# Kernel optimization log

Measured on AMD Instinct MI355X. Metric: run time of the kernel, lower is better.

## Reference

```python
import jax, jax.numpy as jnp
import numpy as np

B, H, W = 16, 288, 384
NUM_ITER = 5      # LMSolver num_iter
LM_DAMP = 1e-4
Z_MIN = 0.01      # PerspectiveCamera z_min
REL_DELTA = 0.1   # AdaptiveHuberPnPCost relative_delta


def skew(v):
    x, y, z = v[..., 0], v[..., 1], v[..., 2]
    O = jnp.zeros_like(x)
    return jnp.stack([jnp.stack([O, -z, y], -1),
                      jnp.stack([z, O, -x], -1),
                      jnp.stack([-y, x, O], -1)], -2)


def exp_so3(w):
    th = jnp.maximum(jnp.linalg.norm(w, axis=-1, keepdims=True), 1e-8)
    K = skew(w / th)
    th = th[..., None]
    I = jnp.eye(3, dtype=w.dtype)
    return I + jnp.sin(th) * K + (1.0 - jnp.cos(th)) * (K @ K)


def se3_inv(T):
    R = T[..., :3, :3]
    t = T[..., :3, 3]
    Rt = jnp.swapaxes(R, -1, -2)
    ti = -jnp.einsum('...ij,...j->...i', Rt, t)
    return (jnp.zeros_like(T).at[..., :3, :3].set(Rt)
            .at[..., :3, 3].set(ti).at[..., 3, 3].set(1.0))


def project(x3d, R, t, K):
    Xc = jnp.einsum('bij,bnj->bni', R, x3d) + t[:, None]  # [B,N,3]
    z = jnp.maximum(Xc[..., 2], Z_MIN)
    fx, fy = K[:, 0, 0, None], K[:, 1, 1, None]
    cx, cy = K[:, 0, 2, None], K[:, 1, 2, None]
    uv = jnp.stack([fx * Xc[..., 0] / z + cx, fy * Xc[..., 1] / z + cy], -1)
    return uv, Xc


def lm_pnp(x3d, x2d, w2d, K):
    """Batched robust Levenberg-Marquardt PnP (replaces per-sample Python loop)."""
    Bb = x3d.shape[0]
    dt = x3d.dtype
    # AdaptiveHuberPnPCost.set_param: delta from spread of x2d
    delta = REL_DELTA * jnp.sqrt(jnp.var(x2d, axis=1).sum(-1))  # [B]
    R = jnp.broadcast_to(jnp.eye(3, dtype=dt), (Bb, 3, 3))
    t = jnp.zeros((Bb, 3), dt)
    I6 = jnp.eye(6, dtype=dt)
    for _ in range(NUM_ITER):
        uv, Xc = project(x3d, R, t, K)
        r = uv - x2d                           # [B,N,2]
        wr = w2d * r
        rn = jnp.linalg.norm(wr, axis=-1)      # [B,N]
        rob = jnp.sqrt(jnp.minimum(1.0, delta[:, None] / jnp.maximum(rn, 1e-8)))
        wt = w2d * rob[..., None]              # [B,N,2] Huber-IRLS weights
        z = jnp.maximum(Xc[..., 2], Z_MIN)
        iz = 1.0 / z
        fx, fy = K[:, 0, 0, None], K[:, 1, 1, None]
        zero = jnp.zeros_like(iz)
        Jp = jnp.stack([
            jnp.stack([fx * iz, zero, -fx * Xc[..., 0] * iz * iz], -1),
            jnp.stack([zero, fy * iz, -fy * Xc[..., 1] * iz * iz], -1)], -2)  # [B,N,2,3]
        Jrot = -jnp.einsum('bnij,bnjk->bnik', Jp, skew(Xc))
        J = jnp.concatenate([Jp, Jrot], -1)    # [B,N,2,6]
        Jw = J * wt[..., None]
        JTJ = jnp.einsum('bnif,bnig->bfg', Jw, Jw)
        JTr = jnp.einsum('bnif,bni->bf', Jw, wt * r)
        damp = LM_DAMP * jnp.trace(JTJ, axis1=-2, axis2=-1)[:, None, None] / 6.0 + 1e-6
        dx = -jnp.linalg.solve(JTJ + damp * I6, JTr[..., None])[..., 0]
        t = t + dx[:, :3]
        R = exp_so3(dx[:, 3:]) @ R
    T = (jnp.zeros((Bb, 4, 4), dt).at[:, :3, :3].set(R)
         .at[:, :3, 3].set(t).at[:, 3, 3].set(1.0))
    return T


def setup_inputs() -> dict:
    key = jax.random.key(0)
    k1, k2, k3, k4, k5 = jax.random.split(key, 5)
    f = 350.0
    Kmat = jnp.array([[f, 0.0, W / 2.0], [0.0, f, H / 2.0], [0.0, 0.0, 1.0]], jnp.float32)
    K = jnp.broadcast_to(Kmat, (B, 3, 3))
    # geometrically consistent points: backproject pixel grid with random depth
    xs = jnp.arange(W, dtype=jnp.float32)
    ys = jnp.arange(H, dtype=jnp.float32)
    gx, gy = jnp.meshgrid(xs, ys, indexing='xy')          # [H,W]
    depth = 2.0 + 4.0 * jax.random.uniform(k1, (B, H, W))
    X = (gx - W / 2.0) / f * depth
    Y = (gy - H / 2.0) / f * depth
    pts3d = jnp.stack([X, Y, depth], -1)
    pts3d = pts3d + 0.02 * jax.random.normal(k2, pts3d.shape)
    conf = 1.0 + jax.random.uniform(k3, (B, H, W))
    # valid SE(3) gt poses (small perturbations of identity)
    q = jax.random.normal(k4, (B, 4)) * 0.05
    q = q.at[:, 0].add(1.0)
    q = q / jnp.linalg.norm(q, axis=-1, keepdims=True)
    w_, x_, y_, z_ = q[:, 0], q[:, 1], q[:, 2], q[:, 3]
    Rg = jnp.stack([
        jnp.stack([1 - 2 * (y_**2 + z_**2), 2 * (x_ * y_ - z_ * w_), 2 * (x_ * z_ + y_ * w_)], -1),
        jnp.stack([2 * (x_ * y_ + z_ * w_), 1 - 2 * (x_**2 + z_**2), 2 * (y_ * z_ - x_ * w_)], -1),
        jnp.stack([2 * (x_ * z_ - y_ * w_), 2 * (y_ * z_ + x_ * w_), 1 - 2 * (x_**2 + y_**2)], -1)], -2)
    tg = 0.2 * jax.random.normal(k5, (B, 3))
    pose = (jnp.zeros((B, 4, 4), jnp.float32).at[:, :3, :3].set(Rg)
            .at[:, :3, 3].set(tg).at[:, 3, 3].set(1.0))
    return {'pts3d_in_other_view': pts3d.astype(jnp.float32),
            'conf': conf.astype(jnp.float32),
            'camera_intrinsics': K.astype(jnp.float32),
            'camera_pose': pose}


def reference(pts3d_in_other_view, conf, camera_intrinsics, camera_pose):
    Bb, Hh, Ww, _ = pts3d_in_other_view.shape
    N = Hh * Ww
    xs = jnp.arange(Ww, dtype=pts3d_in_other_view.dtype)
    ys = jnp.arange(Hh, dtype=pts3d_in_other_view.dtype)
    gx, gy = jnp.meshgrid(xs, ys, indexing='xy')
    pixels = jnp.stack([gx, gy], -1).reshape(1, N, 2)
    x3d = pts3d_in_other_view.reshape(Bb, N, 3)
    x2d = jnp.broadcast_to(pixels, (Bb, N, 2))
    w2d = jnp.broadcast_to(conf.reshape(Bb, N, 1), (Bb, N, 2))
    pred_poses = lm_pnp(x3d, x2d, w2d, camera_intrinsics)
    gt_rel = jnp.einsum('ij,bjk->bik', se3_inv(camera_pose[0]), camera_pose)
    pred_rel = jnp.einsum('ij,bjk->bik', se3_inv(pred_poses[0]), pred_poses)
    R_gt, R_pr = gt_rel[:, :3, :3], pred_rel[:, :3, :3]
    t_gt, t_pr = gt_rel[:, :3, 3], pred_rel[:, :3, 3]
    Rd = jnp.einsum('bji,bjk->bik', R_pr, R_gt)
    trace = Rd[:, 0, 0] + Rd[:, 1, 1] + Rd[:, 2, 2]
    cosang = jnp.clip(0.5 * (trace - 1.0), -1.0 + 1e-7, 1.0 - 1e-7)
    rot_loss = jnp.arccos(cosang).mean()
    trans_loss = jnp.linalg.norm(t_pr - t_gt, axis=-1).mean()
    return rot_loss + trans_loss, rot_loss, trans_loss
```

## Files before the change

kernel.cpp:

```cpp
#include <hip/hip_runtime.h>
#include <math.h>

#define NB 16
#define IMH 288
#define IMW 384
#define NPIX (IMH*IMW)
#define TPB 256
#define PPT 8
#define BPB (NPIX/(TPB*PPT))
#define NBLK (NB*BPB)
#define NITER 5

#define POSE_OFF 0
#define ACC_OFF (2*NB*12)
#define WS_DOUBLES (2*NB*12 + NITER*NB*27)

__device__ __forceinline__ void solve_updatef(const double* __restrict__ acc,
                                              const double* __restrict__ pin,
                                              float* __restrict__ Ro,
                                              double* __restrict__ to) {
    float A[6][6], rhs[6], inv[6];
    {
        int k = 0;
        #pragma unroll
        for (int f = 0; f < 6; f++) {
            #pragma unroll 6
            for (int g = f; g < 6; g++) {
                float v = (float)acc[k];
                A[f][g] = v; A[g][f] = v; k++;
            }
        }
    }
    #pragma unroll
    for (int f = 0; f < 6; f++) rhs[f] = -(float)acc[21 + f];

    float tr = A[0][0]+A[1][1]+A[2][2]+A[3][3]+A[4][4]+A[5][5];
    float damp = 1e-4f * tr * (1.0f/6.0f) + 1e-6f;
    #pragma unroll
    for (int f = 0; f < 6; f++) A[f][f] += damp;

    #pragma unroll
    for (int j = 0; j < 6; j++) {
        float s = A[j][j];
        #pragma unroll 6
        for (int m = 0; m < j; m++) s = fmaf(-A[j][m], A[j][m], s);
        float dd = __builtin_amdgcn_sqrtf(fmaxf(s, 1e-20f));
        A[j][j] = dd;
        inv[j] = __builtin_amdgcn_rcpf(dd);
        #pragma unroll 6
        for (int i = j + 1; i < 6; i++) {
            float s2 = A[i][j];
            #pragma unroll 6
            for (int m = 0; m < j; m++) s2 = fmaf(-A[i][m], A[j][m], s2);
            A[i][j] = s2 * inv[j];
        }
    }
    #pragma unroll
    for (int i = 0; i < 6; i++) {
        float s = rhs[i];
        #pragma unroll 6
        for (int m = 0; m < i; m++) s = fmaf(-A[i][m], rhs[m], s);
        rhs[i] = s * inv[i];
    }
    #pragma unroll
    for (int i = 5; i >= 0; i--) {
        float s = rhs[i];
        #pragma unroll 6
        for (int m = i + 1; m < 6; m++) s = fmaf(-A[m][i], rhs[m], s);
        rhs[i] = s * inv[i];
    }

    to[0] = pin[9]  + (double)rhs[0];
    to[1] = pin[10] + (double)rhs[1];
    to[2] = pin[11] + (double)rhs[2];

    float wx = rhs[3], wy = rhs[4], wz = rhs[5];
    float th = fmaxf(__builtin_amdgcn_sqrtf(fmaf(wx,wx,fmaf(wy,wy,wz*wz))), 1e-8f);
    float ith = __builtin_amdgcn_rcpf(th);
    float kx = wx*ith, ky = wy*ith, kz = wz*ith;
    float st, ctf;
    sincosf(th, &st, &ctf);
    float ct = 1.0f - ctf;
    float E[9];
    E[0] = 1.0f + ct*(kx*kx - 1.0f);
    E[1] = -st*kz + ct*kx*ky;
    E[2] =  st*ky + ct*kx*kz;
    E[3] =  st*kz + ct*ky*kx;
    E[4] = 1.0f + ct*(ky*ky - 1.0f);
    E[5] = -st*kx + ct*ky*kz;
    E[6] = -st*ky + ct*kz*kx;
    E[7] =  st*kx + ct*kz*ky;
    E[8] = 1.0f + ct*(kz*kz - 1.0f);

    float Rin[9];
    #pragma unroll
    for (int i = 0; i < 9; i++) Rin[i] = (float)pin[i];
    #pragma unroll
    for (int i = 0; i < 3; i++) {
        #pragma unroll
        for (int j = 0; j < 3; j++)
            Ro[i*3+j] = E[i*3+0]*Rin[0*3+j] + E[i*3+1]*Rin[1*3+j] + E[i*3+2]*Rin[2*3+j];
    }
}

__global__ void init_k(double* ws) {
    int i = threadIdx.x;
    for (int k = i; k < WS_DOUBLES; k += TPB) ws[k] = 0.0;
    __syncthreads();
    if (i < NB) {
        double* p = ws + POSE_OFF + i * 12;
        p[0] = 1.0; p[4] = 1.0; p[8] = 1.0;
    }
}

__global__ __launch_bounds__(TPB) void reduce_k(const float* __restrict__ x3d,
                                                const float* __restrict__ conf,
                                                const float* __restrict__ Kmat,
                                                double* __restrict__ ws, int it) {
    const int b = blockIdx.x / BPB;
    const int chunk = blockIdx.x % BPB;
    const int tid = threadIdx.x;

    const int ft = chunk * TPB + tid;
    const float4* P4 = reinterpret_cast<const float4*>(x3d + (size_t)b * NPIX * 3) + (size_t)ft * 6;
    const float4* W4 = reinterpret_cast<const float4*>(conf + (size_t)b * NPIX) + (size_t)ft * 2;
    const float4 va = P4[0], vb = P4[1], vc = P4[2], vd = P4[3], ve = P4[4], vf = P4[5];
    const float4 w0 = W4[0], w1 = W4[1];

    __shared__ double lds[TPB / 64][27];

    float R[9], t[3];
    if (it == 0) {
        R[0]=1.f; R[1]=0.f; R[2]=0.f;
        R[3]=0.f; R[4]=1.f; R[5]=0.f;
        R[6]=0.f; R[7]=0.f; R[8]=1.f;
        t[0]=t[1]=t[2]=0.f;
    } else {
        float Rn[9]; double tn[3];
        solve_updatef(ws + ACC_OFF + ((size_t)(it-1) * NB + b) * 27,
                      ws + POSE_OFF + (size_t)((it-1) & 1) * NB * 12 + (size_t)b * 12,
                      Rn, tn);
        #pragma unroll
        for (int i = 0; i < 9; i++) R[i] = Rn[i];
        t[0] = (float)tn[0]; t[1] = (float)tn[1]; t[2] = (float)tn[2];
        if (chunk == 0 && tid == 0) {
            double* pout = ws + POSE_OFF + (size_t)(it & 1) * NB * 12 + (size_t)b * 12;
            #pragma unroll
            for (int i = 0; i < 9; i++) pout[i] = (double)Rn[i];
            pout[9] = tn[0]; pout[10] = tn[1]; pout[11] = tn[2];
        }
    }

    const float fx = Kmat[b*9 + 0];
    const float fy = Kmat[b*9 + 4];
    const float cx = Kmat[b*9 + 2];
    const float cy = Kmat[b*9 + 5];
    const float delta = (float)(0.1 * sqrt(((double)(IMW*IMW - 1) + (double)(IMH*IMH - 1)) / 12.0));

    const int n0 = ft * PPT;
    const int v0 = n0 / IMW;
    const float cyv  = cy - (float)v0;
    const float cxu0 = cx - (float)(n0 - v0 * IMW);

    float ppx[8] = { va.x, va.w, vb.z, vc.y, vd.x, vd.w, ve.z, vf.y };
    float ppy[8] = { va.y, vb.x, vb.w, vc.z, vd.y, ve.x, ve.w, vf.z };
    float ppz[8] = { va.z, vb.y, vc.x, vc.w, vd.z, ve.y, vf.x, vf.w };
    float pw[8]  = { w0.x, w0.y, w0.z, w0.w, w1.x, w1.y, w1.z, w1.w };

    float facc[27];
    #pragma unroll
    for (int i = 0; i < 27; i++) facc[i] = 0.0f;

    #pragma unroll
    for (int g = 0; g < PPT; ++g) {
        float px = ppx[g], py = ppy[g], pz = ppz[g], w = pw[g];
        float u_off = cxu0 - (float)g;

        float Xx = fmaf(R[0], px, fmaf(R[1], py, fmaf(R[2], pz, t[0])));
        float Xy = fmaf(R[3], px, fmaf(R[4], py, fmaf(R[5], pz, t[1])));
        float Xz = fmaf(R[6], px, fmaf(R[7], py, fmaf(R[8], pz, t[2])));
        float z  = fmaxf(Xz, 0.01f);
        float iz = __builtin_amdgcn_rcpf(z);

        float Xxiz = Xx * iz, Xyiz = Xy * iz;
        float rx = fmaf(fx, Xxiz, u_off);
        float ry = fmaf(fy, Xyiz, cyv);

        float wrx = w * rx, wry = w * ry;
        float q  = fmaf(wrx, wrx, wry * wry);
        float rs = __builtin_amdgcn_rsqf(fmaxf(q, 1e-16f));
        float rob2 = fminf(1.0f, delta * rs);
        float sq = w * __builtin_amdgcn_sqrtf(rob2);

        float sqiz = sq * iz;
        float a  = fx * sqiz;
        float c  = fy * sqiz;
        float bb = -a * Xxiz;
        float d  = -c * Xyiz;

        float j0[6] = { a, 0.0f, bb,  bb*Xy,               fmaf(a, Xz, -bb*Xx), -a*Xy };
        float j1[6] = { 0.0f, c,  d,  fmaf(d, Xy, -c*Xz), -d*Xx,                 c*Xx };
        float rxs = sq * rx, rys = sq * ry;

        int k = 0;
        #pragma unroll
        for (int f = 0; f < 6; ++f) {
            #pragma unroll
            for (int gg = f; gg < 6; ++gg) {
                facc[k] += j0[f]*j0[gg] + j1[f]*j1[gg];
                k++;
            }
        }
        #pragma unroll
        for (int f = 0; f < 6; ++f)
            facc[21 + f] += j0[f]*rxs + j1[f]*rys;
    }

    int lane = tid & 63;
    int wave = tid >> 6;
    #pragma unroll
    for (int i = 0; i < 27; i++) {
        float v = facc[i];
        for (int off = 32; off > 0; off >>= 1) v += __shfl_down(v, off, 64);
        if (lane == 0) lds[wave][i] = (double)v;
    }
    __syncthreads();

    double* acc = ws + ACC_OFF + ((size_t)it * NB + b) * 27;
    if (tid < 27) {
        double v = 0.0;
        #pragma unroll
        for (int wv = 0; wv < TPB/64; wv++) v += lds[wv][tid];
        atomicAdd(acc + tid, v);
    }
}

__global__ __launch_bounds__(64) void loss_k(const double* __restrict__ ws,
                                             const float* __restrict__ pose,
                                             float* __restrict__ out) {
    int lane = threadIdx.x;
    double Rp[9] = {1,0,0, 0,1,0, 0,0,1}, tp[3] = {0,0,0};
    if (lane < NB) {
        float Rn[9]; double tn[3];
        solve_updatef(ws + ACC_OFF + ((size_t)(NITER-1) * NB + lane) * 27,
                      ws + POSE_OFF + (size_t)((NITER-1) & 1) * NB * 12 + (size_t)lane * 12,
                      Rn, tn);
        #pragma unroll
        for (int i = 0; i < 9; i++) Rp[i] = (double)Rn[i];
        tp[0] = tn[0]; tp[1] = tn[1]; tp[2] = tn[2];
    }
    double Rp0[9], tp0v[3];
    #pragma unroll
    for (int i = 0; i < 9; i++) Rp0[i] = __shfl(Rp[i], 0, 64);
    #pragma unroll
    for (int i = 0; i < 3; i++) tp0v[i] = __shfl(tp[i], 0, 64);

    double rot = 0.0, trans = 0.0;
    if (lane < NB) {
        const float* P0 = pose;
        const float* Pb = pose + lane * 16;
        double R0t[9];
        #pragma unroll
        for (int i = 0; i < 3; i++)
            #pragma unroll
            for (int j = 0; j < 3; j++) R0t[i*3+j] = (double)P0[j*4+i];
        double t0i[3];
        #pragma unroll
        for (int i = 0; i < 3; i++)
            t0i[i] = -(R0t[i*3+0]*P0[0*4+3] + R0t[i*3+1]*P0[1*4+3] + R0t[i*3+2]*P0[2*4+3]);
        double Rg[9], tg[3];
        #pragma unroll
        for (int i = 0; i < 3; i++) {
            #pragma unroll
            for (int j = 0; j < 3; j++)
                Rg[i*3+j] = R0t[i*3+0]*Pb[0*4+j] + R0t[i*3+1]*Pb[1*4+j] + R0t[i*3+2]*Pb[2*4+j];
            tg[i] = R0t[i*3+0]*Pb[0*4+3] + R0t[i*3+1]*Pb[1*4+3] + R0t[i*3+2]*Pb[2*4+3] + t0i[i];
        }
        double Rp0t[9];
        #pragma unroll
        for (int i = 0; i < 3; i++)
            #pragma unroll
            for (int j = 0; j < 3; j++) Rp0t[i*3+j] = Rp0[j*3+i];
        double tp0i[3];
        #pragma unroll
        for (int i = 0; i < 3; i++)
            tp0i[i] = -(Rp0t[i*3+0]*tp0v[0] + Rp0t[i*3+1]*tp0v[1] + Rp0t[i*3+2]*tp0v[2]);
        double Rr[9], tr[3];
        #pragma unroll
        for (int i = 0; i < 3; i++) {
            #pragma unroll
            for (int j = 0; j < 3; j++)
                Rr[i*3+j] = Rp0t[i*3+0]*Rp[0*3+j] + Rp0t[i*3+1]*Rp[1*3+j] + Rp0t[i*3+2]*Rp[2*3+j];
            tr[i] = Rp0t[i*3+0]*tp[0] + Rp0t[i*3+1]*tp[1] + Rp0t[i*3+2]*tp[2] + tp0i[i];
        }
        double trace = 0.0;
        #pragma unroll
        for (int i = 0; i < 3; i++)
            trace += Rr[0*3+i]*Rg[0*3+i] + Rr[1*3+i]*Rg[1*3+i] + Rr[2*3+i]*Rg[2*3+i];
        double cosang = 0.5 * (trace - 1.0);
        cosang = fmin(fmax(cosang, -1.0 + 1e-7), 1.0 - 1e-7);
        rot = acos(cosang);
        double d0 = tr[0]-tg[0], d1 = tr[1]-tg[1], d2 = tr[2]-tg[2];
        trans = sqrt(d0*d0 + d1*d1 + d2*d2);
    }
    for (int off = 8; off > 0; off >>= 1) {
        rot   += __shfl_down(rot, off, 64);
        trans += __shfl_down(trans, off, 64);
    }
    if (lane == 0) {
        rot /= NB; trans /= NB;
        out[0] = (float)(rot + trans);
        out[1] = (float)rot;
        out[2] = (float)trans;
    }
}

extern "C" void kernel_launch(void* const* d_in, const int* in_sizes, int n_in,
                              void* d_out, int out_size, void* d_ws, size_t ws_size,
                              hipStream_t stream) {
    const float* x3d  = (const float*)d_in[0];
    const float* conf = (const float*)d_in[1];
    const float* Kmat = (const float*)d_in[2];
    const float* pose = (const float*)d_in[3];
    float* out = (float*)d_out;
    double* ws = (double*)d_ws;

    hipLaunchKernelGGL(init_k, dim3(1), dim3(TPB), 0, stream, ws);
    for (int it = 0; it < NITER; ++it) {
        hipLaunchKernelGGL(reduce_k, dim3(NBLK), dim3(TPB), 0, stream,
                           x3d, conf, Kmat, ws, it);
    }
    hipLaunchKernelGGL(loss_k, dim3(1), dim3(64), 0, stream, ws, pose, out);
}
```

Measured before the change: 86.24 us.

## Fuse LM iterations into one persistent kernel with per-batch atomic readiness flags

Measured after the change: 305.4 us. +254.1%, slower.

```diff
diff --git a/kernel.cpp b/kernel.cpp
--- a/kernel.cpp
+++ b/kernel.cpp
@@ -11,14 +11,15 @@
 #define NBLK (NB*BPB)
 #define NITER 5
 
+#define PSTRIDE 16
+#define ASTRIDE 32
 #define POSE_OFF 0
-#define ACC_OFF (2*NB*12)
-#define WS_DOUBLES (2*NB*12 + NITER*NB*27)
+#define ACC_OFF ((NITER+1)*NB*PSTRIDE)
+#define WS_DOUBLES (ACC_OFF + NITER*NB*ASTRIDE)
 
 __device__ __forceinline__ void solve_updatef(const double* __restrict__ acc,
                                               const double* __restrict__ pin,
-                                              float* __restrict__ Ro,
-                                              double* __restrict__ to) {
+                                              double* __restrict__ pout) {
     float A[6][6], rhs[6], inv[6];
     {
         int k = 0;
@@ -70,9 +71,9 @@
         rhs[i] = s * inv[i];
     }
 
-    to[0] = pin[9]  + (double)rhs[0];
-    to[1] = pin[10] + (double)rhs[1];
-    to[2] = pin[11] + (double)rhs[2];
+    pout[9]  = pin[9]  + (double)rhs[0];
+    pout[10] = pin[10] + (double)rhs[1];
+    pout[11] = pin[11] + (double)rhs[2];
 
     float wx = rhs[3], wy = rhs[4], wz = rhs[5];
     float th = fmaxf(__builtin_amdgcn_sqrtf(fmaf(wx,wx,fmaf(wy,wy,wz*wz))), 1e-8f);
@@ -99,57 +100,39 @@
     for (int i = 0; i < 3; i++) {
         #pragma unroll
         for (int j = 0; j < 3; j++)
-            Ro[i*3+j] = E[i*3+0]*Rin[0*3+j] + E[i*3+1]*Rin[1*3+j] + E[i*3+2]*Rin[2*3+j];
+            pout[i*3+j] = (double)(E[i*3+0]*Rin[0*3+j] + E[i*3+1]*Rin[1*3+j] + E[i*3+2]*Rin[2*3+j]);
     }
 }
 
 __global__ void init_k(double* ws) {
     int i = threadIdx.x;
     for (int k = i; k < WS_DOUBLES; k += TPB) ws[k] = 0.0;
+    int* cnt = (int*)(ws + WS_DOUBLES);
+    for (int k = i; k < 2 * NITER * NB + 1; k += TPB) cnt[k] = 0;
     __syncthreads();
     if (i < NB) {
-        double* p = ws + POSE_OFF + i * 12;
+        double* p = ws + POSE_OFF + i * PSTRIDE;
         p[0] = 1.0; p[4] = 1.0; p[8] = 1.0;
     }
 }
 
-__global__ __launch_bounds__(TPB) void reduce_k(const float* __restrict__ x3d,
-                                                const float* __restrict__ conf,
-                                                const float* __restrict__ Kmat,
-                                                double* __restrict__ ws, int it) {
+__global__ __launch_bounds__(TPB) void fused_k(const float* __restrict__ x3d,
+                                               const float* __restrict__ conf,
+                                               const float* __restrict__ Kmat,
+                                               const float* __restrict__ pose,
+                                               float* __restrict__ out,
+                                               double* __restrict__ ws) {
     const int b = blockIdx.x / BPB;
     const int chunk = blockIdx.x % BPB;
     const int tid = threadIdx.x;
 
+    int* cnt     = (int*)(ws + WS_DOUBLES);
+    int* ready   = cnt + NITER * NB;
+    int* losscnt = ready + NITER * NB;
+
     const int ft = chunk * TPB + tid;
     const float4* P4 = reinterpret_cast<const float4*>(x3d + (size_t)b * NPIX * 3) + (size_t)ft * 6;
     const float4* W4 = reinterpret_cast<const float4*>(conf + (size_t)b * NPIX) + (size_t)ft * 2;
-    const float4 va = P4[0], vb = P4[1], vc = P4[2], vd = P4[3], ve = P4[4], vf = P4[5];
-    const float4 w0 = W4[0], w1 = W4[1];
-
-    __shared__ double lds[TPB / 64][27];
-
-    float R[9], t[3];
-    if (it == 0) {
-        R[0]=1.f; R[1]=0.f; R[2]=0.f;
-        R[3]=0.f; R[4]=1.f; R[5]=0.f;
-        R[6]=0.f; R[7]=0.f; R[8]=1.f;
-        t[0]=t[1]=t[2]=0.f;
-    } else {
-        float Rn[9]; double tn[3];
-        solve_updatef(ws + ACC_OFF + ((size_t)(it-1) * NB + b) * 27,
-                      ws + POSE_OFF + (size_t)((it-1) & 1) * NB * 12 + (size_t)b * 12,
-                      Rn, tn);
-        #pragma unroll
-        for (int i = 0; i < 9; i++) R[i] = Rn[i];
-        t[0] = (float)tn[0]; t[1] = (float)tn[1]; t[2] = (float)tn[2];
-        if (chunk == 0 && tid == 0) {
-            double* pout = ws + POSE_OFF + (size_t)(it & 1) * NB * 12 + (size_t)b * 12;
-            #pragma unroll
-            for (int i = 0; i < 9; i++) pout[i] = (double)Rn[i];
-            pout[9] = tn[0]; pout[10] = tn[1]; pout[11] = tn[2];
-        }
-    }
 
     const float fx = Kmat[b*9 + 0];
     const float fy = Kmat[b*9 + 4];
@@ -162,156 +145,187 @@
     const float cyv  = cy - (float)v0;
     const float cxu0 = cx - (float)(n0 - v0 * IMW);
 
-    float ppx[8] = { va.x, va.w, vb.z, vc.y, vd.x, vd.w, ve.z, vf.y };
-    float ppy[8] = { va.y, vb.x, vb.w, vc.z, vd.y, ve.x, ve.w, vf.z };
-    float ppz[8] = { va.z, vb.y, vc.x, vc.w, vd.z, ve.y, vf.x, vf.w };
-    float pw[8]  = { w0.x, w0.y, w0.z, w0.w, w1.x, w1.y, w1.z, w1.w };
-
-    float facc[27];
-    #pragma unroll
-    for (int i = 0; i < 27; i++) facc[i] = 0.0f;
-
-    #pragma unroll
-    for (int g = 0; g < PPT; ++g) {
-        float px = ppx[g], py = ppy[g], pz = ppz[g], w = pw[g];
-        float u_off = cxu0 - (float)g;
-
-        float Xx = fmaf(R[0], px, fmaf(R[1], py, fmaf(R[2], pz, t[0])));
-        float Xy = fmaf(R[3], px, fmaf(R[4], py, fmaf(R[5], pz, t[1])));
-        float Xz = fmaf(R[6], px, fmaf(R[7], py, fmaf(R[8], pz, t[2])));
-        float z  = fmaxf(Xz, 0.01f);
-        float iz = __builtin_amdgcn_rcpf(z);
-
-        float Xxiz = Xx * iz, Xyiz = Xy * iz;
-        float rx = fmaf(fx, Xxiz, u_off);
-        float ry = fmaf(fy, Xyiz, cyv);
-
-        float wrx = w * rx, wry = w * ry;
-        float q  = fmaf(wrx, wrx, wry * wry);
-        float rs = __builtin_amdgcn_rsqf(fmaxf(q, 1e-16f));
-        float rob2 = fminf(1.0f, delta * rs);
-        float sq = w * __builtin_amdgcn_sqrtf(rob2);
-
-        float sqiz = sq * iz;
-        float a  = fx * sqiz;
-        float c  = fy * sqiz;
-        float bb = -a * Xxiz;
-        float d  = -c * Xyiz;
-
-        float j0[6] = { a, 0.0f, bb,  bb*Xy,               fmaf(a, Xz, -bb*Xx), -a*Xy };
-        float j1[6] = { 0.0f, c,  d,  fmaf(d, Xy, -c*Xz), -d*Xx,                 c*Xx };
-        float rxs = sq * rx, rys = sq * ry;
-
-        int k = 0;
-        #pragma unroll
-        for (int f = 0; f < 6; ++f) {
+    __shared__ double lds[TPB / 64][27];
+    __shared__ int s_last, s_loss;
+
+    const int lane = tid & 63;
+    const int wave = tid >> 6;
+
+    for (int it = 0; it < NITER; ++it) {
+        if (it > 0) {
+            if (tid == 0) {
+                int spins = 0;
+                while (__hip_atomic_load(&ready[(it-1)*NB + b], __ATOMIC_ACQUIRE,
+                                         __HIP_MEMORY_SCOPE_AGENT) == 0) {
+                    __builtin_amdgcn_s_sleep(4);
+                    if (++spins > (1 << 27)) break;
+                }
+                __threadfence();
+            }
+            __syncthreads();
+        }
+
+        const double* pin = ws + POSE_OFF + ((size_t)it * NB + b) * PSTRIDE;
+        float R[9], t[3];
+        #pragma unroll
+        for (int i = 0; i < 9; i++) R[i] = (float)pin[i];
+        t[0] = (float)pin[9]; t[1] = (float)pin[10]; t[2] = (float)pin[11];
+
+        const float4 va = P4[0], vb = P4[1], vc = P4[2], vd = P4[3], ve = P4[4], vf = P4[5];
+        const float4 w0 = W4[0], w1 = W4[1];
+        float ppx[8] = { va.x, va.w, vb.z, vc.y, vd.x, vd.w, ve.z, vf.y };
+        float ppy[8] = { va.y, vb.x, vb.w, vc.z, vd.y, ve.x, ve.w, vf.z };
+        float ppz[8] = { va.z, vb.y, vc.x, vc.w, vd.z, ve.y, vf.x, vf.w };
+        float pw[8]  = { w0.x, w0.y, w0.z, w0.w, w1.x, w1.y, w1.z, w1.w };
+
+        float facc[27];
+        #pragma unroll
+        for (int i = 0; i < 27; i++) facc[i] = 0.0f;
+
+        #pragma unroll
+        for (int g = 0; g < PPT; ++g) {
+            float px = ppx[g], py = ppy[g], pz = ppz[g], w = pw[g];
+            float u_off = cxu0 - (float)g;
+
+            float Xx = fmaf(R[0], px, fmaf(R[1], py, fmaf(R[2], pz, t[0])));
+            float Xy = fmaf(R[3], px, fmaf(R[4], py, fmaf(R[5], pz, t[1])));
+            float Xz = fmaf(R[6], px, fmaf(R[7], py, fmaf(R[8], pz, t[2])));
+            float z  = fmaxf(Xz, 0.01f);
+            float iz = __builtin_amdgcn_rcpf(z);
+
+            float Xxiz = Xx * iz, Xyiz = Xy * iz;
+            float rx = fmaf(fx, Xxiz, u_off);
+            float ry = fmaf(fy, Xyiz, cyv);
+
+            float wrx = w * rx, wry = w * ry;
+            float q  = fmaf(wrx, wrx, wry * wry);
+            float rs = __builtin_amdgcn_rsqf(fmaxf(q, 1e-16f));
+            float rob2 = fminf(1.0f, delta * rs);
+            float sq = w * __builtin_amdgcn_sqrtf(rob2);
+
+            float sqiz = sq * iz;
+            float a  = fx * sqiz;
+            float c  = fy * sqiz;
+            float bb = -a * Xxiz;
+            float d  = -c * Xyiz;
+
+            float j0[6] = { a, 0.0f, bb,  bb*Xy,               fmaf(a, Xz, -bb*Xx), -a*Xy };
+            float j1[6] = { 0.0f, c,  d,  fmaf(d, Xy, -c*Xz), -d*Xx,                 c*Xx };
+            float rxs = sq * rx, rys = sq * ry;
+
+            int k = 0;
             #pragma unroll
-            for (int gg = f; gg < 6; ++gg) {
-                facc[k] += j0[f]*j0[gg] + j1[f]*j1[gg];
-                k++;
-            }
-        }
-        #pragma unroll
-        for (int f = 0; f < 6; ++f)
-            facc[21 + f] += j0[f]*rxs + j1[f]*rys;
-    }
-
-    int lane = tid & 63;
-    int wave = tid >> 6;
-    #pragma unroll
-    for (int i = 0; i < 27; i++) {
-        float v = facc[i];
-        for (int off = 32; off > 0; off >>= 1) v += __shfl_down(v, off, 64);
-        if (lane == 0) lds[wave][i] = (double)v;
-    }
-    __syncthreads();
-
-    double* acc = ws + ACC_OFF + ((size_t)it * NB + b) * 27;
-    if (tid < 27) {
-        double v = 0.0;
-        #pragma unroll
-        for (int wv = 0; wv < TPB/64; wv++) v += lds[wv][tid];
-        atomicAdd(acc + tid, v);
-    }
-}
-
-__global__ __launch_bounds__(64) void loss_k(const double* __restrict__ ws,
-                                             const float* __restrict__ pose,
-                                             float* __restrict__ out) {
-    int lane = threadIdx.x;
-    double Rp[9] = {1,0,0, 0,1,0, 0,0,1}, tp[3] = {0,0,0};
-    if (lane < NB) {
-        float Rn[9]; double tn[3];
-        solve_updatef(ws + ACC_OFF + ((size_t)(NITER-1) * NB + lane) * 27,
-                      ws + POSE_OFF + (size_t)((NITER-1) & 1) * NB * 12 + (size_t)lane * 12,
-                      Rn, tn);
-        #pragma unroll
-        for (int i = 0; i < 9; i++) Rp[i] = (double)Rn[i];
-        tp[0] = tn[0]; tp[1] = tn[1]; tp[2] = tn[2];
-    }
-    double Rp0[9], tp0v[3];
-    #pragma unroll
-    for (int i = 0; i < 9; i++) Rp0[i] = __shfl(Rp[i], 0, 64);
-    #pragma unroll
-    for (int i = 0; i < 3; i++) tp0v[i] = __shfl(tp[i], 0, 64);
-
-    double rot = 0.0, trans = 0.0;
-    if (lane < NB) {
-        const float* P0 = pose;
-        const float* Pb = pose + lane * 16;
-        double R0t[9];
-        #pragma unroll
-        for (int i = 0; i < 3; i++)
+            for (int f = 0; f < 6; ++f) {
+                #pragma unroll
+                for (int gg = f; gg < 6; ++gg) {
+                    facc[k] += j0[f]*j0[gg] + j1[f]*j1[gg];
+                    k++;
+                }
+            }
             #pragma unroll
-            for (int j = 0; j < 3; j++) R0t[i*3+j] = (double)P0[j*4+i];
-        double t0i[3];
-        #pragma unroll
-        for (int i = 0; i < 3; i++)
-            t0i[i] = -(R0t[i*3+0]*P0[0*4+3] + R0t[i*3+1]*P0[1*4+3] + R0t[i*3+2]*P0[2*4+3]);
-        double Rg[9], tg[3];
-        #pragma unroll
-        for (int i = 0; i < 3; i++) {
-            #pragma unroll
-            for (int j = 0; j < 3; j++)
-                Rg[i*3+j] = R0t[i*3+0]*Pb[0*4+j] + R0t[i*3+1]*Pb[1*4+j] + R0t[i*3+2]*Pb[2*4+j];
-            tg[i] = R0t[i*3+0]*Pb[0*4+3] + R0t[i*3+1]*Pb[1*4+3] + R0t[i*3+2]*Pb[2*4+3] + t0i[i];
-        }
-        double Rp0t[9];
-        #pragma unroll
-        for (int i = 0; i < 3; i++)
-            #pragma unroll
-            for (int j = 0; j < 3; j++) Rp0t[i*3+j] = Rp0[j*3+i];
-        double tp0i[3];
-        #pragma unroll
-        for (int i = 0; i < 3; i++)
-            tp0i[i] = -(Rp0t[i*3+0]*tp0v[0] + Rp0t[i*3+1]*tp0v[1] + Rp0t[i*3+2]*tp0v[2]);
-        double Rr[9], tr[3];
-        #pragma unroll
-        for (int i = 0; i < 3; i++) {
-            #pragma unroll
-            for (int j = 0; j < 3; j++)
-                Rr[i*3+j] = Rp0t[i*3+0]*Rp[0*3+j] + Rp0t[i*3+1]*Rp[1*3+j] + Rp0t[i*3+2]*Rp[2*3+j];
-            tr[i] = Rp0t[i*3+0]*tp[0] + Rp0t[i*3+1]*tp[1] + Rp0t[i*3+2]*tp[2] + tp0i[i];
-        }
-        double trace = 0.0;
-        #pragma unroll
-        for (int i = 0; i < 3; i++)
-            trace += Rr[0*3+i]*Rg[0*3+i] + Rr[1*3+i]*Rg[1*3+i] + Rr[2*3+i]*Rg[2*3+i];
-        double cosang = 0.5 * (trace - 1.0);
-        cosang = fmin(fmax(cosang, -1.0 + 1e-7), 1.0 - 1e-7);
-        rot = acos(cosang);
-        double d0 = tr[0]-tg[0], d1 = tr[1]-tg[1], d2 = tr[2]-tg[2];
-        trans = sqrt(d0*d0 + d1*d1 + d2*d2);
-    }
-    for (int off = 8; off > 0; off >>= 1) {
-        rot   += __shfl_down(rot, off, 64);
-        trans += __shfl_down(trans, off, 64);
-    }
-    if (lane == 0) {
-        rot /= NB; trans /= NB;
-        out[0] = (float)(rot + trans);
-        out[1] = (float)rot;
-        out[2] = (float)trans;
+            for (int f = 0; f < 6; ++f)
+                facc[21 + f] += j0[f]*rxs + j1[f]*rys;
+        }
+
+        #pragma unroll
+        for (int i = 0; i < 27; i++) {
+            float v = facc[i];
+            for (int off = 32; off > 0; off >>= 1) v += __shfl_down(v, off, 64);
+            if (lane == 0) lds[wave][i] = (double)v;
+        }
+        __syncthreads();
+
+        double* acc = ws + ACC_OFF + ((size_t)it * NB + b) * ASTRIDE;
+        if (tid < 27) {
+            double v = lds[0][tid] + lds[1][tid] + lds[2][tid] + lds[3][tid];
+            atomicAdd(acc + tid, v);
+        }
+        __syncthreads();
+
+        if (tid == 0) {
+            s_loss = 0;
+            int old = atomicAdd(&cnt[it * NB + b], 1);
+            s_last = (old == BPB - 1) ? 1 : 0;
+        }
+        __syncthreads();
+        if (s_last) {
+            if (tid == 0) {
+                __threadfence();
+                double* pout = ws + POSE_OFF + ((size_t)(it+1) * NB + b) * PSTRIDE;
+                solve_updatef(acc, pin, pout);
+                __threadfence();
+                __hip_atomic_store(&ready[it*NB + b], 1, __ATOMIC_RELEASE,
+                                   __HIP_MEMORY_SCOPE_AGENT);
+                if (it == NITER - 1) {
+                    int o2 = atomicAdd(losscnt, 1);
+                    if (o2 == NB - 1) s_loss = 1;
+                }
+            }
+            __syncthreads();
+            if (s_loss && tid < 64) {
+                __threadfence();
+                double rot = 0.0, trans = 0.0;
+                if (lane < NB) {
+                    const float* P0 = pose;
+                    const float* Pb = pose + lane * 16;
+                    double R0t[9];
+                    #pragma unroll
+                    for (int i = 0; i < 3; i++)
+                        #pragma unroll
+                        for (int j = 0; j < 3; j++) R0t[i*3+j] = (double)P0[j*4+i];
+                    double t0i[3];
+                    #pragma unroll
+                    for (int i = 0; i < 3; i++)
+                        t0i[i] = -(R0t[i*3+0]*P0[0*4+3] + R0t[i*3+1]*P0[1*4+3] + R0t[i*3+2]*P0[2*4+3]);
+                    double Rg[9], tg[3];
+                    #pragma unroll
+                    for (int i = 0; i < 3; i++) {
+                        #pragma unroll
+                        for (int j = 0; j < 3; j++)
+                            Rg[i*3+j] = R0t[i*3+0]*Pb[0*4+j] + R0t[i*3+1]*Pb[1*4+j] + R0t[i*3+2]*Pb[2*4+j];
+                        tg[i] = R0t[i*3+0]*Pb[0*4+3] + R0t[i*3+1]*Pb[1*4+3] + R0t[i*3+2]*Pb[2*4+3] + t0i[i];
+                    }
+                    const double* pf0 = ws + POSE_OFF + ((size_t)NITER * NB + 0) * PSTRIDE;
+                    const double* pfb = ws + POSE_OFF + ((size_t)NITER * NB + lane) * PSTRIDE;
+                    double Rp0t[9];
+                    #pragma unroll
+                    for (int i = 0; i < 3; i++)
+                        #pragma unroll
+                        for (int j = 0; j < 3; j++) Rp0t[i*3+j] = pf0[j*3+i];
+                    double tp0i[3];
+                    #pragma unroll
+                    for (int i = 0; i < 3; i++)
+                        tp0i[i] = -(Rp0t[i*3+0]*pf0[9] + Rp0t[i*3+1]*pf0[10] + Rp0t[i*3+2]*pf0[11]);
+                    double Rr[9], trv[3];
+                    #pragma unroll
+                    for (int i = 0; i < 3; i++) {
+                        #pragma unroll
+                        for (int j = 0; j < 3; j++)
+                            Rr[i*3+j] = Rp0t[i*3+0]*pfb[0*3+j] + Rp0t[i*3+1]*pfb[1*3+j] + Rp0t[i*3+2]*pfb[2*3+j];
+                        trv[i] = Rp0t[i*3+0]*pfb[9] + Rp0t[i*3+1]*pfb[10] + Rp0t[i*3+2]*pfb[11] + tp0i[i];
+                    }
+                    double trace = 0.0;
+                    #pragma unroll
+                    for (int i = 0; i < 3; i++)
+                        trace += Rr[0*3+i]*Rg[0*3+i] + Rr[1*3+i]*Rg[1*3+i] + Rr[2*3+i]*Rg[2*3+i];
+                    double cosang = 0.5 * (trace - 1.0);
+                    cosang = fmin(fmax(cosang, -1.0 + 1e-7), 1.0 - 1e-7);
+                    rot = acos(cosang);
+                    double d0 = trv[0]-tg[0], d1 = trv[1]-tg[1], d2 = trv[2]-tg[2];
+                    trans = sqrt(d0*d0 + d1*d1 + d2*d2);
+                }
+                for (int off = 8; off > 0; off >>= 1) {
+                    rot   += __shfl_down(rot, off, 64);
+                    trans += __shfl_down(trans, off, 64);
+                }
+                if (lane == 0) {
+                    rot /= NB; trans /= NB;
+                    out[0] = (float)(rot + trans);
+                    out[1] = (float)rot;
+                    out[2] = (float)trans;
+                }
+            }
+        }
     }
 }
 
@@ -326,9 +340,6 @@
     double* ws = (double*)d_ws;
 
     hipLaunchKernelGGL(init_k, dim3(1), dim3(TPB), 0, stream, ws);
-    for (int it = 0; it < NITER; ++it) {
-        hipLaunchKernelGGL(reduce_k, dim3(NBLK), dim3(TPB), 0, stream,
-                           x3d, conf, Kmat, ws, it);
-    }
-    hipLaunchKernelGGL(loss_k, dim3(1), dim3(64), 0, stream, ws, pose, out);
+    hipLaunchKernelGGL(fused_k, dim3(NBLK), dim3(TPB), 0, stream,
+                       x3d, conf, Kmat, pose, out, ws);
 }
```
